# Optimization experiments

Measured on AMD Instinct MI355X. Metric: run time of the kernel, lower is better.

## Reference

```python
import jax, jax.numpy as jnp
import numpy as np


def _apply_1q(state, U, wire):
    # state: (B,) + (2,)*n big-endian (wire 0 = axis 1, Pennylane convention)
    # U: (2,2) shared or (B,2,2) per-sample
    s = jnp.moveaxis(state, wire + 1, 1)
    eq = 'bij,bj...->bi...' if U.ndim == 3 else 'ij,bj...->bi...'
    s = jnp.einsum(eq, U, s)
    return jnp.moveaxis(s, 1, wire + 1)


def _rx(theta):  # theta: (B,) -> (B,2,2)
    c = jnp.cos(theta / 2).astype(jnp.complex64)
    s = (-1j * jnp.sin(theta / 2)).astype(jnp.complex64)
    return jnp.stack([jnp.stack([c, s], -1), jnp.stack([s, c], -1)], -2)


def _ry(theta):  # theta: (B,) -> (B,2,2)
    c = jnp.cos(theta / 2).astype(jnp.complex64)
    s = jnp.sin(theta / 2).astype(jnp.complex64)
    return jnp.stack([jnp.stack([c, -s], -1), jnp.stack([s, c], -1)], -2)


def _rot(phi, theta, omega):  # Pennylane Rot = RZ(omega) RY(theta) RZ(phi)
    c = jnp.cos(theta / 2)
    s = jnp.sin(theta / 2)
    r0 = jnp.stack([jnp.exp(-1j * (phi + omega) / 2) * c,
                    -jnp.exp(1j * (phi - omega) / 2) * s])
    r1 = jnp.stack([jnp.exp(-1j * (phi - omega) / 2) * s,
                    jnp.exp(1j * (phi + omega) / 2) * c])
    return jnp.stack([r0, r1]).astype(jnp.complex64)


def _cnot_adj(state, ctrl):
    # CNOT(control=ctrl, target=ctrl+1): flip target axis on control=1 slice
    a0 = jax.lax.index_in_dim(state, 0, ctrl + 1, keepdims=True)
    a1 = jax.lax.index_in_dim(state, 1, ctrl + 1, keepdims=True)
    return jnp.concatenate([a0, jnp.flip(a1, axis=ctrl + 2)], axis=ctrl + 1)


def _forward(state_batch, weights, head_w, head_b):
    L, n, _ = weights.shape
    B = state_batch.shape[0]
    psi = jnp.zeros((B, 2 ** n), jnp.complex64).at[:, 0].set(1.0)
    psi = psi.reshape((B,) + (2,) * n)
    # angle encoding (only first two features are used, as in the torch module)
    psi = _apply_1q(psi, _rx(state_batch[:, 0]), 0)
    psi = _apply_1q(psi, _ry(state_batch[:, 1]), 1)
    for l in range(L):
        for w in range(n):
            psi = _apply_1q(psi, _rot(weights[l, w, 0], weights[l, w, 1], weights[l, w, 2]), w)
        for i in range(n - 1):
            psi = _cnot_adj(psi, i)
    probs = psi.real ** 2 + psi.imag ** 2  # (B,) + (2,)*n
    feats = []
    for w in range(n):  # expval PauliZ on each wire
        p = probs.sum(axis=tuple(a for a in range(1, n + 1) if a != w + 1))
        feats.append(p[:, 0] - p[:, 1])
    features = jnp.stack(feats, axis=-1)  # (B, n)
    return (features @ head_w.T + head_b).squeeze(-1)  # (B,)


def setup_inputs() -> dict:
    key = jax.random.key(0)
    k1, k2, k3 = jax.random.split(key, 3)
    B, n, L = 8192, 12, 8
    return {
        'state_batch': jax.random.normal(k1, (B, 8), jnp.float32),
        'weights': jax.random.normal(k2, (L, n, 3), jnp.float32),
        'head_w': jax.random.normal(k3, (1, n), jnp.float32) / np.float32(np.sqrt(n)),
        'head_b': jnp.zeros((1,), jnp.float32),
    }


def reference(state_batch, weights, head_w, head_b):
    return _forward(state_batch, weights, head_w, head_b)
```

## Files before the change

### kernel.cpp

```cpp
#include <hip/hip_runtime.h>
#include <hip/hip_fp16.h>


typedef __half2 h2;
typedef _Float16 f16;
typedef __attribute__((ext_vector_type(8))) _Float16 f16x8;
typedef __attribute__((ext_vector_type(16))) float f32x16;

struct Gate32 { float a, b, c, d; };

#define SGN2 0x80008000
#define Z16 f32x16{0,0,0,0,0,0,0,0,0,0,0,0,0,0,0,0}

__device__ __forceinline__ float bpermf(int addr4, float v) {
    return __int_as_float(__builtin_amdgcn_ds_bpermute(addr4, __float_as_int(v)));
}
__device__ __forceinline__ int bci(h2 v)  { return __builtin_bit_cast(int, v); }
__device__ __forceinline__ h2 bch2(int v) { return __builtin_bit_cast(h2, v); }
__device__ __forceinline__ int g6(int x)  { return (x ^ (x >> 1)) & 63; }
__device__ __forceinline__ int moff(int row, int unit) {
    return row * 128 + ((unit ^ (row & 7)) << 4);
}
__device__ __forceinline__ f16x8 fneg8(f16x8 v) {
    int4 x = __builtin_bit_cast(int4, v);
    x.x ^= SGN2; x.y ^= SGN2; x.z ^= SGN2; x.w ^= SGN2;
    return __builtin_bit_cast(f16x8, x);
}
__device__ __forceinline__ f32x16 MFMA(f16x8 a, f16x8 b, f32x16 c) {
    return __builtin_amdgcn_mfma_f32_32x32x16_f16(a, b, c, 0, 0, 0);
}

struct C2 { float r, i; };
__device__ __forceinline__ C2 cmul(C2 x, C2 y) {
    return { x.r*y.r - x.i*y.i, x.r*y.i + x.i*y.r };
}
__device__ __forceinline__ C2 gent(const Gate32 g, int bi, int bj) {
    const float re = (bi == bj) ? g.a : (bi ? g.c : -g.c);
    const float im = (bi == bj) ? (bi ? g.b : -g.b) : -g.d;
    return { re, im };
}

__global__ __launch_bounds__(256, 1)
void sim_kernel(const float* __restrict__ wts, float2* __restrict__ cols) {
    extern __shared__ char smem[];
    char* Sr = smem + 65536;
    char* Si = smem + 73728;
    char* Ur = smem + 81920;
    char* Ui = smem + 90112;
    float* KLr = (float*)(smem + 98304);
    float* KLi = KLr + 64;  float* KRr = KLr + 128; float* KRi = KLr + 192;
    f16* KLpr = (f16*)(smem + 99328);
    f16* KLpi = KLpr + 64;  f16* KRpr = KLpr + 128; f16* KRpi = KLpr + 192;
    Gate32* gt = (Gate32*)(smem + 99840);

    const int tid  = threadIdx.x;
    const int lane = tid & 63;
    const int wid  = tid >> 6;
    const int b    = blockIdx.x;
    const int lo5  = lane & 31, hi = (lane >> 5) & 1;

    if (tid < 96) {
        const int l = tid / 12, w = tid % 12;
        const float* lw = wts + l*36 + w*3;
        float ch, sh, ca, sa, cb, sb_;
        __sincosf(0.5f*lw[1],         &sh, &ch);
        __sincosf(0.5f*(lw[0]+lw[2]), &sa, &ca);
        __sincosf(0.5f*(lw[0]-lw[2]), &sb_, &cb);
        Gate32 r; r.a = ca*ch; r.b = sa*ch; r.c = cb*sh; r.d = sb_*sh;
        gt[tid] = r;
    }
    {
        const int4 z = make_int4(0, 0, 0, 0);
#pragma unroll
        for (int u = 0; u < 2; ++u) {
            const int idx = u * 256 + tid;
            const int row = idx >> 3, un = idx & 7;
            *(int4*)(Sr + moff(row, un)) = z;
            *(int4*)(Si + moff(row, un)) = z;
        }
    }
    __syncthreads();
    if (tid == 0) {
        const int row = 16 * b;
        *(f16*)(Sr + moff(row, 0)) = (f16)1.0f;
    }
    if (tid < 64) {
        const Gate32* gl = gt;
        const int ip = tid >> 3, jp = tid & 7;
        const int i2 = (ip>>2)&1, i1 = (ip>>1)&1, i0 = ip&1;
        const int j2 = (jp>>2)&1, j1 = (jp>>1)&1, j0 = jp&1;
        const C2 kl  = cmul(cmul(gent(gl[0],i2,j2), gent(gl[1],i1,j1)), gent(gl[2],i0,j0));
        const C2 klp = cmul(cmul(gent(gl[3],i2,j2), gent(gl[4],i1,j1)), gent(gl[5],i0,j0));
        const C2 kr  = cmul(cmul(gent(gl[6],i2,j2), gent(gl[7],i1,j1)), gent(gl[8],i0,j0));
        const C2 krp = cmul(cmul(gent(gl[9],i2,j2), gent(gl[10],i1,j1)), gent(gl[11],i0,j0));
        KLr[tid] = kl.r;  KLi[tid] = kl.i;
        KRr[tid] = kr.r;  KRi[tid] = kr.i;
        KLpr[tid] = (f16)klp.r;  KLpi[tid] = (f16)klp.i;
        KRpr[tid] = (f16)krp.r;  KRpi[tid] = (f16)krp.i;
    }
    __syncthreads();

#pragma unroll 1
    for (int l = 0; l < 8; ++l) {
        char* Lr = smem + (l & 1) * 32768;
        char* Li = Lr + 8192;
        char* Rr = Lr + 16384;
        char* Ri = Lr + 24576;
        {
            const int r = tid & 63, rh = r >> 3, rl = r & 7;
            const int side = (tid >> 6) & 1;
            const int hsel = tid >> 7;
            const float* xr4 = side ? (KRr + rh*8) : (KLr + rh*8);
            const float* xi4 = side ? (KRi + rh*8) : (KLi + rh*8);
            const int4 pyr = *(const int4*)((side ? KRpr : KLpr) + rl*8);
            const int4 pyi = *(const int4*)((side ? KRpi : KLpi) + rl*8);
            const h2 yr[4] = { bch2(pyr.x), bch2(pyr.y), bch2(pyr.z), bch2(pyr.w) };
            const h2 yi[4] = { bch2(pyi.x), bch2(pyi.y), bch2(pyi.z), bch2(pyi.w) };
            char* Pr = side ? Rr : Lr;
            char* Pi = side ? Ri : Li;
#pragma unroll
            for (int q = 0; q < 4; ++q) {
                const int hk = 4*hsel + q;
                const h2 xr2  = __float2half2_rn(xr4[hk]);
                const h2 xi2  = __float2half2_rn(xi4[hk]);
                const h2 nxi2 = bch2(bci(xi2) ^ SGN2);
                h2 oR[4], oI[4];
#pragma unroll
                for (int t = 0; t < 4; ++t) {
                    oR[t] = __hfma2(nxi2, yi[t], __hmul2(xr2, yr[t]));
                    oI[t] = __hfma2(xi2,  yr[t], __hmul2(xr2, yi[t]));
                }
                *(int4*)(Pr + moff(r, hk)) = make_int4(bci(oR[0]), bci(oR[1]), bci(oR[2]), bci(oR[3]));
                *(int4*)(Pi + moff(r, hk)) = make_int4(bci(oI[0]), bci(oI[1]), bci(oI[2]), bci(oI[3]));
            }
        }
        __syncthreads();
        {
            const int mt = wid >> 1, nt = wid & 1;
            f16x8 asr[4], asi[4], brr[4], bri[4];
            const int arow = 32*mt + lo5;
            const int brow = g6(32*nt + lo5);
#pragma unroll
            for (int kc = 0; kc < 4; ++kc) {
                const int un = 2*kc + hi;
                asr[kc] = *(const f16x8*)(Sr + moff(arow, un));
                asi[kc] = *(const f16x8*)(Si + moff(arow, un));
                brr[kc] = *(const f16x8*)(Rr + moff(brow, un));
                bri[kc] = *(const f16x8*)(Ri + moff(brow, un));
            }
            f32x16 ur0 = Z16, ur1 = Z16, ui0 = Z16, ui1 = Z16;
#pragma unroll
            for (int kc = 0; kc < 2; ++kc) {
                const f16x8 nri = fneg8(bri[kc]);
                ur0 = MFMA(asr[kc], brr[kc], ur0);
                ur0 = MFMA(asi[kc], nri,     ur0);
                ui0 = MFMA(asr[kc], bri[kc], ui0);
                ui0 = MFMA(asi[kc], brr[kc], ui0);
            }
#pragma unroll
            for (int kc = 2; kc < 4; ++kc) {
                const f16x8 nri = fneg8(bri[kc]);
                ur1 = MFMA(asr[kc], brr[kc], ur1);
                ur1 = MFMA(asi[kc], nri,     ur1);
                ui1 = MFMA(asr[kc], bri[kc], ui1);
                ui1 = MFMA(asi[kc], brr[kc], ui1);
            }
            const int urow = 32*nt + lo5;
#pragma unroll
            for (int gg = 0; gg < 4; ++gg) {
                const h2 p0 = __floats2half2_rn(ur0[4*gg+0]+ur1[4*gg+0], ur0[4*gg+1]+ur1[4*gg+1]);
                const h2 p1 = __floats2half2_rn(ur0[4*gg+2]+ur1[4*gg+2], ur0[4*gg+3]+ur1[4*gg+3]);
                *(int2*)(Ur + moff(urow, 4*mt+gg) + 8*hi) = make_int2(bci(p0), bci(p1));
                const h2 q0 = __floats2half2_rn(ui0[4*gg+0]+ui1[4*gg+0], ui0[4*gg+1]+ui1[4*gg+1]);
                const h2 q1 = __floats2half2_rn(ui0[4*gg+2]+ui1[4*gg+2], ui0[4*gg+3]+ui1[4*gg+3]);
                *(int2*)(Ui + moff(urow, 4*mt+gg) + 8*hi) = make_int2(bci(q0), bci(q1));
            }
            if (l < 7 && tid < 64) {
                const Gate32* gl2 = gt + (l+1) * 12;
                const int ip = tid >> 3, jp = tid & 7;
                const int i2 = (ip>>2)&1, i1 = (ip>>1)&1, i0 = ip&1;
                const int j2 = (jp>>2)&1, j1 = (jp>>1)&1, j0 = jp&1;
                const C2 kl  = cmul(cmul(gent(gl2[0],i2,j2), gent(gl2[1],i1,j1)), gent(gl2[2],i0,j0));
                const C2 klp = cmul(cmul(gent(gl2[3],i2,j2), gent(gl2[4],i1,j1)), gent(gl2[5],i0,j0));
                const C2 kr  = cmul(cmul(gent(gl2[6],i2,j2), gent(gl2[7],i1,j1)), gent(gl2[8],i0,j0));
                const C2 krp = cmul(cmul(gent(gl2[9],i2,j2), gent(gl2[10],i1,j1)), gent(gl2[11],i0,j0));
                KLr[tid] = kl.r;  KLi[tid] = kl.i;
                KRr[tid] = kr.r;  KRi[tid] = kr.i;
                KLpr[tid] = (f16)klp.r;  KLpi[tid] = (f16)klp.i;
                KRpr[tid] = (f16)krp.r;  KRpi[tid] = (f16)krp.i;
            }
        }
        __syncthreads();
        {
            const int nt2 = wid >> 1, mt2 = wid & 1;
            f16x8 a1r[4], a1i[4], a2r[4], a2i[4];
            const int r1 = 32*nt2 + lo5, r2 = r1 ^ 63;
#pragma unroll
            for (int kc = 0; kc < 4; ++kc) {
                const int un = 2*kc + hi;
                a1r[kc] = *(const f16x8*)(Ur + moff(r1, un));
                a1i[kc] = *(const f16x8*)(Ui + moff(r1, un));
                a2r[kc] = *(const f16x8*)(Ur + moff(r2, un));
                a2i[kc] = *(const f16x8*)(Ui + moff(r2, un));
            }
            const int m = 32*mt2 + lo5;
            const int lrow = g6(m);
            f16x8 blr[4], bli[4];
#pragma unroll
            for (int kc = 0; kc < 4; ++kc) {
                const int un = 2*kc + hi;
                blr[kc] = *(const f16x8*)(Lr + moff(lrow, un));
                bli[kc] = *(const f16x8*)(Li + moff(lrow, un));
            }
            f32x16 w1r = Z16, w1i = Z16, w2r = Z16, w2i = Z16;
#pragma unroll
            for (int kc = 0; kc < 4; ++kc) {
                const f16x8 nbli = fneg8(bli[kc]);
                w1r = MFMA(a1r[kc], blr[kc], w1r);
                w1r = MFMA(a1i[kc], nbli,    w1r);
                w1i = MFMA(a1r[kc], bli[kc], w1i);
                w1i = MFMA(a1i[kc], blr[kc], w1i);
                w2r = MFMA(a2r[kc], blr[kc], w2r);
                w2r = MFMA(a2i[kc], nbli,    w2r);
                w2i = MFMA(a2r[kc], bli[kc], w2i);
                w2i = MFMA(a2i[kc], blr[kc], w2i);
            }
            const bool odd = (m & 1);
            if (l < 7) {
#pragma unroll
                for (int gg = 0; gg < 4; ++gg) {
                    float s0 = odd ? w2r[4*gg+0] : w1r[4*gg+0];
                    float s1 = odd ? w2r[4*gg+1] : w1r[4*gg+1];
                    float s2 = odd ? w2r[4*gg+2] : w1r[4*gg+2];
                    float s3 = odd ? w2r[4*gg+3] : w1r[4*gg+3];
                    *(int2*)(Sr + moff(m, 4*nt2+gg) + 8*hi) =
                        make_int2(bci(__floats2half2_rn(s0, s1)),
                                  bci(__floats2half2_rn(s2, s3)));
                    s0 = odd ? w2i[4*gg+0] : w1i[4*gg+0];
                    s1 = odd ? w2i[4*gg+1] : w1i[4*gg+1];
                    s2 = odd ? w2i[4*gg+2] : w1i[4*gg+2];
                    s3 = odd ? w2i[4*gg+3] : w1i[4*gg+3];
                    *(int2*)(Si + moff(m, 4*nt2+gg) + 8*hi) =
                        make_int2(bci(__floats2half2_rn(s0, s1)),
                                  bci(__floats2half2_rn(s2, s3)));
                }
            } else {
#pragma unroll
                for (int gg = 0; gg < 4; ++gg)
#pragma unroll
                for (int e = 0; e < 4; ++e) {
                    const int n = 32*nt2 + 8*gg + 4*hi + e;
                    const int r = 4*gg + e;
                    const float vr = odd ? w2r[r] : w1r[r];
                    const float vi = odd ? w2i[r] : w1i[r];
                    cols[b*4096 + (m << 6) + n] = make_float2(vr, vi);
                }
            }
        }
    }
}

__global__ __launch_bounds__(1024)
void finish_kernel(const float* __restrict__ sb,
                   const float2* __restrict__ cols,
                   const float* __restrict__ hw,
                   const float* __restrict__ hb,
                   float* __restrict__ out, int B) {
    __shared__ float Gsh[10];
    const int tid  = threadIdx.x;
    const int lane = tid & 63;

    if (tid < 10) Gsh[tid] = 0.f;

    float hwv[12];
#pragma unroll
    for (int w = 0; w < 12; ++w) hwv[w] = hw[w];

    float Klo = 0.f;
#pragma unroll
    for (int w = 2; w < 12; ++w)
        Klo += ((tid >> (11 - w)) & 1) ? -hwv[w] : hwv[w];

    __syncthreads();

    float g[10];
#pragma unroll
    for (int m = 0; m < 10; ++m) g[m] = 0.f;

#pragma unroll 1
    for (int it = 0; it < 4; ++it) {
        const int q = (it << 10) | tid;
        const float2 c0 = cols[q];
        const float2 c1 = cols[4096  + q];
        const float2 c2 = cols[8192  + q];
        const float2 c3 = cols[12288 + q];
        float K = Klo;
        K += ((it >> 1) & 1) ? -hwv[0] : hwv[0];
        K += (it & 1)        ? -hwv[1] : hwv[1];
        g[0] += K * (c0.x*c0.x + c0.y*c0.y);
        g[1] += K * (c1.x*c1.x + c1.y*c1.y);
        g[2] += K * (c2.x*c2.x + c2.y*c2.y);
        g[3] += K * (c3.x*c3.x + c3.y*c3.y);
        g[4] += K * (c0.x*c1.x + c0.y*c1.y);
        g[5] += K * (c2.x*c3.x + c2.y*c3.y);
        g[6] += K * (c0.x*c2.y - c0.y*c2.x);
        g[7] += K * (c0.x*c3.y - c0.y*c3.x);
        g[8] += K * (c1.x*c2.y - c1.y*c2.x);
        g[9] += K * (c1.x*c3.y - c1.y*c3.x);
    }

#pragma unroll
    for (int m = 0; m < 10; ++m) {
#pragma unroll
        for (int off = 1; off < 64; off <<= 1)
            g[m] += bpermf((lane ^ off) << 2, g[m]);
    }
#pragma unroll
    for (int m = 0; m < 10; ++m)
        if (lane == m) atomicAdd(&Gsh[m], g[m]);
    __syncthreads();

    float G[10];
#pragma unroll
    for (int m = 0; m < 10; ++m)
        G[m] = ((m < 4) ? 1.f : 2.f) * Gsh[m];

    const int i = blockIdx.x * 1024 + tid;
    if (i < B) {
        const float2 x = *reinterpret_cast<const float2*>(sb + i*8);
        float c0, s0, c1, s1;
        __sincosf(0.5f * x.x, &s0, &c0);
        __sincosf(0.5f * x.y, &s1, &c1);
        const float a0 = c0*c1, a1 = c0*s1, a2 = s0*c1, a3 = s0*s1;
        const float r = G[0]*a0*a0 + G[1]*a1*a1 + G[2]*a2*a2 + G[3]*a3*a3
                      + G[4]*(a0*a1) + G[5]*(a2*a3)
                      + G[6]*(a0*a2) + G[7]*(a0*a3)
                      + G[8]*(a1*a2) + G[9]*(a1*a3);
        out[i] = r + hb[0];
    }
}

extern "C" void kernel_launch(void* const* d_in, const int* in_sizes, int n_in,
                              void* d_out, int out_size, void* d_ws, size_t ws_size,
                              hipStream_t stream) {
    const float* sb  = (const float*)d_in[0];
    const float* wts = (const float*)d_in[1];
    const float* hw  = (const float*)d_in[2];
    const float* hb  = (const float*)d_in[3];
    float* out = (float*)d_out;
    float2* cols = (float2*)((char*)d_ws + 4096);
    const int B = in_sizes[0] / 8;
    sim_kernel   <<<4, 256, 101376, stream>>>(wts, cols);
    finish_kernel<<<(B + 1023)/1024, 1024, 0, stream>>>(sb, cols, hw, hb, out, B);
}
```

Baseline: 88.42 us.

## Double sim_kernel block to 512 threads, splitting MFMA work across wave pairs

Raises the simulation block from 256 to 512 threads (8 waves). In the first GEMM each wave pair now splits the real and imaginary output. In the second GEMM each pair splits the two reflected-row products, and each wave stores only the rows matching its parity. The intent is to halve the serial MFMA chain per wave in this latency-bound kernel, which runs only 4 blocks. The cost is extra redundant A/B fragment loads from shared memory and more waves taking part in each barrier.

```diff
diff --git a/kernel.cpp b/kernel.cpp
--- a/kernel.cpp
+++ b/kernel.cpp
@@ -40,7 +40,7 @@
     return { re, im };
 }
 
-__global__ __launch_bounds__(256, 1)
+__global__ __launch_bounds__(512, 1)
 void sim_kernel(const float* __restrict__ wts, float2* __restrict__ cols) {
     extern __shared__ char smem[];
     char* Sr = smem + 65536;
@@ -71,13 +71,9 @@
     }
     {
         const int4 z = make_int4(0, 0, 0, 0);
-#pragma unroll
-        for (int u = 0; u < 2; ++u) {
-            const int idx = u * 256 + tid;
-            const int row = idx >> 3, un = idx & 7;
-            *(int4*)(Sr + moff(row, un)) = z;
-            *(int4*)(Si + moff(row, un)) = z;
-        }
+        const int row = tid >> 3, un = tid & 7;
+        *(int4*)(Sr + moff(row, un)) = z;
+        *(int4*)(Si + moff(row, un)) = z;
     }
     __syncthreads();
     if (tid == 0) {
@@ -119,8 +115,8 @@
             char* Pr = side ? Rr : Lr;
             char* Pi = side ? Ri : Li;
 #pragma unroll
-            for (int q = 0; q < 4; ++q) {
-                const int hk = 4*hsel + q;
+            for (int q = 0; q < 2; ++q) {
+                const int hk = 2*hsel + q;
                 const h2 xr2  = __float2half2_rn(xr4[hk]);
                 const h2 xi2  = __float2half2_rn(xi4[hk]);
                 const h2 nxi2 = bch2(bci(xi2) ^ SGN2);
@@ -136,8 +132,10 @@
         }
         __syncthreads();
         {
-            const int mt = wid >> 1, nt = wid & 1;
-            f16x8 asr[4], asi[4], brr[4], bri[4];
+            const int tile = wid >> 1;
+            const int mt = tile >> 1, nt = tile & 1;
+            const int ri = wid & 1;
+            f16x8 asr[4], asi[4], bX[4], bY[4];
             const int arow = 32*mt + lo5;
             const int brow = g6(32*nt + lo5);
 #pragma unroll
@@ -145,35 +143,29 @@
                 const int un = 2*kc + hi;
                 asr[kc] = *(const f16x8*)(Sr + moff(arow, un));
                 asi[kc] = *(const f16x8*)(Si + moff(arow, un));
-                brr[kc] = *(const f16x8*)(Rr + moff(brow, un));
-                bri[kc] = *(const f16x8*)(Ri + moff(brow, un));
-            }
-            f32x16 ur0 = Z16, ur1 = Z16, ui0 = Z16, ui1 = Z16;
+                const f16x8 brr = *(const f16x8*)(Rr + moff(brow, un));
+                const f16x8 bri = *(const f16x8*)(Ri + moff(brow, un));
+                bX[kc] = ri ? bri : brr;
+                bY[kc] = ri ? brr : fneg8(bri);
+            }
+            f32x16 u0 = Z16, u1 = Z16;
 #pragma unroll
             for (int kc = 0; kc < 2; ++kc) {
-                const f16x8 nri = fneg8(bri[kc]);
-                ur0 = MFMA(asr[kc], brr[kc], ur0);
-                ur0 = MFMA(asi[kc], nri,     ur0);
-                ui0 = MFMA(asr[kc], bri[kc], ui0);
-                ui0 = MFMA(asi[kc], brr[kc], ui0);
+                u0 = MFMA(asr[kc], bX[kc], u0);
+                u0 = MFMA(asi[kc], bY[kc], u0);
             }
 #pragma unroll
             for (int kc = 2; kc < 4; ++kc) {
-                const f16x8 nri = fneg8(bri[kc]);
-                ur1 = MFMA(asr[kc], brr[kc], ur1);
-                ur1 = MFMA(asi[kc], nri,     ur1);
-                ui1 = MFMA(asr[kc], bri[kc], ui1);
-                ui1 = MFMA(asi[kc], brr[kc], ui1);
-            }
+                u1 = MFMA(asr[kc], bX[kc], u1);
+                u1 = MFMA(asi[kc], bY[kc], u1);
+            }
+            char* Up = ri ? Ui : Ur;
             const int urow = 32*nt + lo5;
 #pragma unroll
             for (int gg = 0; gg < 4; ++gg) {
-                const h2 p0 = __floats2half2_rn(ur0[4*gg+0]+ur1[4*gg+0], ur0[4*gg+1]+ur1[4*gg+1]);
-                const h2 p1 = __floats2half2_rn(ur0[4*gg+2]+ur1[4*gg+2], ur0[4*gg+3]+ur1[4*gg+3]);
-                *(int2*)(Ur + moff(urow, 4*mt+gg) + 8*hi) = make_int2(bci(p0), bci(p1));
-                const h2 q0 = __floats2half2_rn(ui0[4*gg+0]+ui1[4*gg+0], ui0[4*gg+1]+ui1[4*gg+1]);
-                const h2 q1 = __floats2half2_rn(ui0[4*gg+2]+ui1[4*gg+2], ui0[4*gg+3]+ui1[4*gg+3]);
-                *(int2*)(Ui + moff(urow, 4*mt+gg) + 8*hi) = make_int2(bci(q0), bci(q1));
+                const h2 p0 = __floats2half2_rn(u0[4*gg+0]+u1[4*gg+0], u0[4*gg+1]+u1[4*gg+1]);
+                const h2 p1 = __floats2half2_rn(u0[4*gg+2]+u1[4*gg+2], u0[4*gg+3]+u1[4*gg+3]);
+                *(int2*)(Up + moff(urow, 4*mt+gg) + 8*hi) = make_int2(bci(p0), bci(p1));
             }
             if (l < 7 && tid < 64) {
                 const Gate32* gl2 = gt + (l+1) * 12;
@@ -192,68 +184,75 @@
         }
         __syncthreads();
         {
-            const int nt2 = wid >> 1, mt2 = wid & 1;
-            f16x8 a1r[4], a1i[4], a2r[4], a2i[4];
-            const int r1 = 32*nt2 + lo5, r2 = r1 ^ 63;
+            const int unit = wid >> 1;
+            const int nt2 = unit >> 1, mt2 = unit & 1;
+            const int px = wid & 1;
+            const int r0 = 32*nt2 + lo5;
+            const int rr = px ? (r0 ^ 63) : r0;
+            f16x8 axr[4], axi[4], blr[4], bli[4];
 #pragma unroll
             for (int kc = 0; kc < 4; ++kc) {
                 const int un = 2*kc + hi;
-                a1r[kc] = *(const f16x8*)(Ur + moff(r1, un));
-                a1i[kc] = *(const f16x8*)(Ui + moff(r1, un));
-                a2r[kc] = *(const f16x8*)(Ur + moff(r2, un));
-                a2i[kc] = *(const f16x8*)(Ui + moff(r2, un));
+                axr[kc] = *(const f16x8*)(Ur + moff(rr, un));
+                axi[kc] = *(const f16x8*)(Ui + moff(rr, un));
             }
             const int m = 32*mt2 + lo5;
             const int lrow = g6(m);
-            f16x8 blr[4], bli[4];
 #pragma unroll
             for (int kc = 0; kc < 4; ++kc) {
                 const int un = 2*kc + hi;
                 blr[kc] = *(const f16x8*)(Lr + moff(lrow, un));
                 bli[kc] = *(const f16x8*)(Li + moff(lrow, un));
             }
-            f32x16 w1r = Z16, w1i = Z16, w2r = Z16, w2i = Z16;
-#pragma unroll
-            for (int kc = 0; kc < 4; ++kc) {
+            f32x16 wr0 = Z16, wr1 = Z16, wi0 = Z16, wi1 = Z16;
+#pragma unroll
+            for (int kc = 0; kc < 2; ++kc) {
                 const f16x8 nbli = fneg8(bli[kc]);
-                w1r = MFMA(a1r[kc], blr[kc], w1r);
-                w1r = MFMA(a1i[kc], nbli,    w1r);
-                w1i = MFMA(a1r[kc], bli[kc], w1i);
-                w1i = MFMA(a1i[kc], blr[kc], w1i);
-                w2r = MFMA(a2r[kc], blr[kc], w2r);
-                w2r = MFMA(a2i[kc], nbli,    w2r);
-                w2i = MFMA(a2r[kc], bli[kc], w2i);
-                w2i = MFMA(a2i[kc], blr[kc], w2i);
-            }
-            const bool odd = (m & 1);
+                wr0 = MFMA(axr[kc], blr[kc], wr0);
+                wr0 = MFMA(axi[kc], nbli,    wr0);
+                wi0 = MFMA(axr[kc], bli[kc], wi0);
+                wi0 = MFMA(axi[kc], blr[kc], wi0);
+            }
+#pragma unroll
+            for (int kc = 2; kc < 4; ++kc) {
+                const f16x8 nbli = fneg8(bli[kc]);
+                wr1 = MFMA(axr[kc], blr[kc], wr1);
+                wr1 = MFMA(axi[kc], nbli,    wr1);
+                wi1 = MFMA(axr[kc], bli[kc], wi1);
+                wi1 = MFMA(axi[kc], blr[kc], wi1);
+            }
+            const bool mine = ((m & 1) == px);
             if (l < 7) {
-#pragma unroll
-                for (int gg = 0; gg < 4; ++gg) {
-                    float s0 = odd ? w2r[4*gg+0] : w1r[4*gg+0];
-                    float s1 = odd ? w2r[4*gg+1] : w1r[4*gg+1];
-                    float s2 = odd ? w2r[4*gg+2] : w1r[4*gg+2];
-                    float s3 = odd ? w2r[4*gg+3] : w1r[4*gg+3];
-                    *(int2*)(Sr + moff(m, 4*nt2+gg) + 8*hi) =
-                        make_int2(bci(__floats2half2_rn(s0, s1)),
-                                  bci(__floats2half2_rn(s2, s3)));
-                    s0 = odd ? w2i[4*gg+0] : w1i[4*gg+0];
-                    s1 = odd ? w2i[4*gg+1] : w1i[4*gg+1];
-                    s2 = odd ? w2i[4*gg+2] : w1i[4*gg+2];
-                    s3 = odd ? w2i[4*gg+3] : w1i[4*gg+3];
-                    *(int2*)(Si + moff(m, 4*nt2+gg) + 8*hi) =
-                        make_int2(bci(__floats2half2_rn(s0, s1)),
-                                  bci(__floats2half2_rn(s2, s3)));
+                if (mine) {
+#pragma unroll
+                    for (int gg = 0; gg < 4; ++gg) {
+                        const float s0 = wr0[4*gg+0]+wr1[4*gg+0];
+                        const float s1 = wr0[4*gg+1]+wr1[4*gg+1];
+                        const float s2 = wr0[4*gg+2]+wr1[4*gg+2];
+                        const float s3 = wr0[4*gg+3]+wr1[4*gg+3];
+                        *(int2*)(Sr + moff(m, 4*nt2+gg) + 8*hi) =
+                            make_int2(bci(__floats2half2_rn(s0, s1)),
+                                      bci(__floats2half2_rn(s2, s3)));
+                        const float t0 = wi0[4*gg+0]+wi1[4*gg+0];
+                        const float t1 = wi0[4*gg+1]+wi1[4*gg+1];
+                        const float t2 = wi0[4*gg+2]+wi1[4*gg+2];
+                        const float t3 = wi0[4*gg+3]+wi1[4*gg+3];
+                        *(int2*)(Si + moff(m, 4*nt2+gg) + 8*hi) =
+                            make_int2(bci(__floats2half2_rn(t0, t1)),
+                                      bci(__floats2half2_rn(t2, t3)));
+                    }
                 }
             } else {
-#pragma unroll
-                for (int gg = 0; gg < 4; ++gg)
-#pragma unroll
-                for (int e = 0; e < 4; ++e) {
-                    const int n = 32*nt2 + 8*gg + 4*hi + e;
-                    const int r = 4*gg + e;
-                    const float vr = odd ? w2r[r] : w1r[r];
-                    const float vi = odd ? w2i[r] : w1i[r];
-                    cols[b*4096 + (m << 6) + n] = make_float2(vr, vi);
+                if (mine) {
+#pragma unroll
+                    for (int gg = 0; gg < 4; ++gg)
+#pragma unroll
+                    for (int e = 0; e < 4; ++e) {
+                        const int n = 32*nt2 + 8*gg + 4*hi + e;
+                        const int r = 4*gg + e;
+                        cols[b*4096 + (m << 6) + n] =
+                            make_float2(wr0[r]+wr1[r], wi0[r]+wi1[r]);
+                    }
                 }
             }
         }
@@ -350,6 +349,6 @@
     float* out = (float*)d_out;
     float2* cols = (float2*)((char*)d_ws + 4096);
     const int B = in_sizes[0] / 8;
-    sim_kernel   <<<4, 256, 101376, stream>>>(wts, cols);
+    sim_kernel   <<<4, 512, 101376, stream>>>(wts, cols);
     finish_kernel<<<(B + 1023)/1024, 1024, 0, stream>>>(sb, cols, hw, hb, out, B);
 }
```

New measurement: 84.92 us. 4.0% less time.
